# Kernel tuning notes

Hardware: AMD Instinct MI355X
Metric: run time of the kernel (lower is better)

## Reference

```python
import jax, jax.numpy as jnp
import numpy as np

EPS = 1e-12  # torch F.normalize default eps

def _l2norm(x):
    # torch.nn.functional.normalize(x, dim=-1): x / max(||x||_2, eps)
    n = jnp.linalg.norm(x, axis=-1, keepdims=True)
    return x / jnp.maximum(n, EPS)

def setup_inputs() -> dict:
    key = jax.random.key(0)
    ks = jax.random.split(key, 12)
    B, T, D, V, C = 16, 2048, 1024, 32000, 6
    s = 0.02
    text = jax.random.randint(ks[0], (B * T,), 0, V, dtype=jnp.int64)
    offsets = (jnp.arange(B, dtype=jnp.int64) * T)  # uniform-length sequences
    emb = jax.random.normal(ks[1], (V, D), dtype=jnp.float32) * s
    Wq = jax.random.normal(ks[2], (D, D), dtype=jnp.float32) * s
    bq = jnp.zeros((D,), jnp.float32)
    Wk = jax.random.normal(ks[3], (D, D), dtype=jnp.float32) * s
    bk = jnp.zeros((D,), jnp.float32)
    Wv = jax.random.normal(ks[4], (D, D), dtype=jnp.float32) * s
    bv = jnp.zeros((D,), jnp.float32)
    Wfc = jax.random.normal(ks[5], (D, D), dtype=jnp.float32) * s
    bfc = jnp.zeros((D,), jnp.float32)
    Wo = jax.random.normal(ks[6], (C, D), dtype=jnp.float32) * s
    bo = jnp.zeros((C,), jnp.float32)
    return {"text": text, "offsets": offsets, "emb": emb,
            "Wq": Wq, "bq": bq, "Wk": Wk, "bk": bk, "Wv": Wv, "bv": bv,
            "Wfc": Wfc, "bfc": bfc, "Wo": Wo, "bo": bo}

def reference(text, offsets, emb, Wq, bq, Wk, bk, Wv, bv, Wfc, bfc, Wo, bo):
    B = offsets.shape[0]
    T = text.shape[0] // B  # uniform lengths -> pad_sequence == reshape
    D = emb.shape[1]
    tok = text.reshape(B, T)
    x = emb[tok]                                   # [B,T,D]
    q = x @ Wq.T + bq
    k = x @ Wk.T + bk
    v = x @ Wv.T + bv
    scores = jnp.einsum('bqd,bkd->bqk', q, k) / jnp.sqrt(jnp.asarray(D, x.dtype))
    causal = jnp.tril(jnp.ones((T, T), dtype=bool))
    scores = jnp.where(causal[None, :, :], scores, -jnp.inf)
    attn = jax.nn.softmax(scores, axis=-1)
    out = jnp.einsum('bqk,bkd->bqd', attn, v) + x  # residual with embedding
    out = _l2norm(out)
    out = out + (out @ Wfc.T + bfc)                # residual FFN
    out = _l2norm(out)
    last = out[:, -1, :]                           # [B,D]
    return jax.nn.sigmoid(last @ Wo.T + bo)        # [B,num_class]
```

## Files before the change

kernel.cpp:

```cpp
#include <hip/hip_runtime.h>
#include <hip/hip_bf16.h>
#include <math.h>

typedef unsigned short ushort_t;

__device__ __forceinline__ float bf2f(ushort_t u) {
    union { unsigned int i; float f; } v;
    v.i = ((unsigned int)u) << 16;
    return v.f;
}

__device__ __forceinline__ ushort_t f2bf(float f) {
    union { float f; unsigned int i; } v; v.f = f;
    unsigned int lsb = (v.i >> 16) & 1;
    unsigned int r = v.i + 0x7FFF + lsb;
    return (ushort_t)(r >> 16);
}

__device__ __forceinline__ float wave_sum(float acc) {
    #pragma unroll
    for (int off = 32; off >= 1; off >>= 1) acc += __shfl_xor(acc, off, 64);
    return acc;
}

__device__ __forceinline__ void ld8(const void* p, int isbf, size_t i, float* o) {
    if (isbf) {
        uint4 raw = *reinterpret_cast<const uint4*>((const ushort_t*)p + i);
        const ushort_t* pu = reinterpret_cast<const ushort_t*>(&raw);
        #pragma unroll
        for (int k = 0; k < 8; ++k) o[k] = bf2f(pu[k]);
    } else {
        const float4* f = reinterpret_cast<const float4*>((const float*)p + i);
        float4 a = f[0], b = f[1];
        o[0]=a.x; o[1]=a.y; o[2]=a.z; o[3]=a.w;
        o[4]=b.x; o[5]=b.y; o[6]=b.z; o[7]=b.w;
    }
}

__device__ __forceinline__ void ld4(const void* p, int isbf, size_t i, float* o) {
    if (isbf) {
        uint2 raw = *reinterpret_cast<const uint2*>((const ushort_t*)p + i);
        const ushort_t* pu = reinterpret_cast<const ushort_t*>(&raw);
        #pragma unroll
        for (int k = 0; k < 4; ++k) o[k] = bf2f(pu[k]);
    } else {
        float4 a = *reinterpret_cast<const float4*>((const float*)p + i);
        o[0]=a.x; o[1]=a.y; o[2]=a.z; o[3]=a.w;
    }
}

__device__ __forceinline__ float ldS(const void* p, int isbf, size_t i) {
    return isbf ? bf2f(((const ushort_t*)p)[i]) : ((const float*)p)[i];
}

__device__ __forceinline__ int tokAt(const void* text, int isi64, size_t i) {
    return isi64 ? ((const int*)text)[2 * i] : ((const int*)text)[i];
}

__device__ __forceinline__ void detect_flags(const void* emb, const void* text, int* sf) {
    if (threadIdx.x < 64) {
        const int lane = threadIdx.x;
        ushort_t u = ((const ushort_t*)emb)[2 * lane];
        int e = (u >> 7) & 0xFF;
        unsigned long long mb = __ballot(e >= 0x60 && e <= 0x7E);
        int odd = ((const int*)text)[2 * lane + 1];
        unsigned long long mi = __ballot(odd != 0);
        if (lane == 0) {
            sf[0] = (__popcll(mb) >= 32) ? 1 : 0;
            sf[1] = (__popcll(mi) == 0) ? 1 : 0;
        }
    }
    __syncthreads();
}

__global__ void kQC(const void* __restrict__ text, const void* __restrict__ emb,
                    const void* __restrict__ Wq, const void* __restrict__ bq,
                    const void* __restrict__ Wk, float* __restrict__ c_part,
                    int B, int T, int D) {
    const int nch = D >> 6;
    const int b = blockIdx.x / nch;
    const int ch = blockIdx.x % nch;
    const int i0 = ch << 6;
    const int tid = threadIdx.x;
    __shared__ int sf[2];
    __shared__ float xs[1024];
    __shared__ float qs[64];
    detect_flags(emb, text, sf);
    const int isbf = sf[0], isi64 = sf[1];
    const int tok = tokAt(text, isi64, (size_t)b * T + (T - 1));
    float w4[4];
    for (int dd = tid * 4; dd < D; dd += 1024) {
        ld4(emb, isbf, (size_t)tok * D + dd, w4);
        xs[dd]=w4[0]; xs[dd+1]=w4[1]; xs[dd+2]=w4[2]; xs[dd+3]=w4[3];
    }
    __syncthreads();
    const int wave = tid >> 6, lane = tid & 63;
    float w[8];
    for (int r = 0; r < 16; ++r) {
        const int i = i0 + wave * 16 + r;
        float acc = 0.f;
        for (int d0 = lane * 8; d0 < D; d0 += 512) {
            ld8(Wq, isbf, (size_t)i * D + d0, w);
            #pragma unroll
            for (int k = 0; k < 8; ++k) acc += w[k] * xs[d0 + k];
        }
        acc = wave_sum(acc);
        if (lane == 0) qs[wave * 16 + r] = acc + ldS(bq, isbf, i);
    }
    __syncthreads();
    const int d = tid * 4;
    float a0=0.f, a1=0.f, a2=0.f, a3=0.f;
    #pragma unroll 8
    for (int i = 0; i < 64; ++i) {
        const float qv = qs[i];
        ld4(Wk, isbf, (size_t)(i0 + i) * D + d, w4);
        a0 += qv*w4[0]; a1 += qv*w4[1]; a2 += qv*w4[2]; a3 += qv*w4[3];
    }
    *reinterpret_cast<float4*>(c_part + ((size_t)ch * B + b) * D + d)
        = make_float4(a0, a1, a2, a3);
}

__global__ void k35(const void* __restrict__ text, const void* __restrict__ emb,
                    const float* __restrict__ c_part, float* __restrict__ xbar_part,
                    float* __restrict__ m_part, float* __restrict__ l_part,
                    int B, int T, int D, int nch_c, float scale) {
    const int nch = T >> 6;
    const int b = blockIdx.x / nch;
    const int ch = blockIdx.x % nch;
    const int j0 = ch << 6;
    const int tid = threadIdx.x;
    __shared__ int sf[2];
    __shared__ float cs[1024];
    __shared__ float sjs[64];
    __shared__ float wls[64];
    __shared__ int tks[64];
    detect_flags(emb, text, sf);
    const int isbf = sf[0], isi64 = sf[1];
    {
        const int d = tid * 4;
        float4 acc = make_float4(0.f, 0.f, 0.f, 0.f);
        for (int cc = 0; cc < nch_c; ++cc) {
            float4 v = *reinterpret_cast<const float4*>(c_part + ((size_t)cc * B + b) * D + d);
            acc.x += v.x; acc.y += v.y; acc.z += v.z; acc.w += v.w;
        }
        cs[d]=acc.x; cs[d+1]=acc.y; cs[d+2]=acc.z; cs[d+3]=acc.w;
    }
    if (tid < 64) tks[tid] = tokAt(text, isi64, (size_t)b * T + j0 + tid);
    __syncthreads();
    const int wave = tid >> 6, lane = tid & 63;
    float w[8];
    for (int r = 0; r < 16; ++r) {
        const int jj = wave * 16 + r;
        const int tok = tks[jj];
        float acc = 0.f;
        for (int d0 = lane * 8; d0 < D; d0 += 512) {
            ld8(emb, isbf, (size_t)tok * D + d0, w);
            #pragma unroll
            for (int k = 0; k < 8; ++k) acc += w[k] * cs[d0 + k];
        }
        acc = wave_sum(acc);
        if (lane == 0) sjs[jj] = acc * scale;
    }
    __syncthreads();
    float mx = -INFINITY;
    #pragma unroll 8
    for (int j = 0; j < 64; ++j) mx = fmaxf(mx, sjs[j]);
    if (tid < 64) wls[tid] = expf(sjs[tid] - mx);
    __syncthreads();
    if (tid < 64) {
        float lv = wave_sum(wls[tid]);
        if (tid == 0) { m_part[ch * B + b] = mx; l_part[ch * B + b] = lv; }
    }
    const int d = tid * 4;
    float a0=0.f, a1=0.f, a2=0.f, a3=0.f;
    float w4[4];
    #pragma unroll 8
    for (int j = 0; j < 64; ++j) {
        const float wj = wls[j];
        ld4(emb, isbf, (size_t)tks[j] * D + d, w4);
        a0 += wj*w4[0]; a1 += wj*w4[1]; a2 += wj*w4[2]; a3 += wj*w4[3];
    }
    *reinterpret_cast<float4*>(xbar_part + ((size_t)ch * B + b) * D + d)
        = make_float4(a0, a1, a2, a3);
}

__global__ void kC(const float* __restrict__ xbar_part, const float* __restrict__ m_part,
                   const float* __restrict__ l_part, float* __restrict__ xbar,
                   int B, int D, int nch) {
    const int b = blockIdx.x >> 2;
    const int d = ((blockIdx.x & 3) << 8) + threadIdx.x;
    float mx = -INFINITY;
    for (int cc = 0; cc < nch; ++cc) mx = fmaxf(mx, m_part[cc * B + b]);
    float lg = 0.f, acc = 0.f;
    for (int cc = 0; cc < nch; ++cc) {
        const float sc = expf(m_part[cc * B + b] - mx);
        lg  += l_part[cc * B + b] * sc;
        acc += xbar_part[((size_t)cc * B + b) * D + d] * sc;
    }
    xbar[b * D + d] = acc / lg;
}

__global__ void k6a_u(const void* __restrict__ text, const void* __restrict__ emb,
                      const void* __restrict__ Wv, const void* __restrict__ bv,
                      const float* __restrict__ xbar, float* __restrict__ u,
                      int B, int T, int D) {
    const int nb = D >> 2;
    const int b = blockIdx.x / nb;
    const int r0 = (blockIdx.x % nb) << 2;
    const int tid = threadIdx.x;
    __shared__ int sf[2];
    __shared__ float xb[1024];
    __shared__ float xl[1024];
    detect_flags(emb, text, sf);
    const int isbf = sf[0], isi64 = sf[1];
    const int tok = tokAt(text, isi64, (size_t)b * T + (T - 1));
    float w4[4];
    for (int dd = tid * 4; dd < D; dd += 1024) {
        float4 v = *reinterpret_cast<const float4*>(xbar + b * D + dd);
        xb[dd]=v.x; xb[dd+1]=v.y; xb[dd+2]=v.z; xb[dd+3]=v.w;
        ld4(emb, isbf, (size_t)tok * D + dd, w4);
        xl[dd]=w4[0]; xl[dd+1]=w4[1]; xl[dd+2]=w4[2]; xl[dd+3]=w4[3];
    }
    __syncthreads();
    const int wave = tid >> 6, lane = tid & 63;
    const int i = r0 + wave;
    float acc = 0.f, w[8];
    for (int d0 = lane * 8; d0 < D; d0 += 512) {
        ld8(Wv, isbf, (size_t)i * D + d0, w);
        #pragma unroll
        for (int k = 0; k < 8; ++k) acc += w[k] * xb[d0 + k];
    }
    acc = wave_sum(acc);
    if (lane == 0) u[b * D + i] = acc + ldS(bv, isbf, i) + xl[i];
}

__global__ void k6c_h2(const void* __restrict__ text, const void* __restrict__ emb,
                       const void* __restrict__ Wfc, const void* __restrict__ bfc,
                       const float* __restrict__ u, float* __restrict__ h2, int D) {
    const int nb = D >> 2;
    const int b = blockIdx.x / nb;
    const int r0 = (blockIdx.x % nb) << 2;
    const int tid = threadIdx.x;
    __shared__ int sf[2];
    __shared__ float hs[1024];
    __shared__ float red[256];
    __shared__ float s_rn;
    detect_flags(emb, text, sf);
    const int isbf = sf[0];
    float part = 0.f;
    for (int dd = tid * 4; dd < D; dd += 1024) {
        float4 v = *reinterpret_cast<const float4*>(u + b * D + dd);
        hs[dd]=v.x; hs[dd+1]=v.y; hs[dd+2]=v.z; hs[dd+3]=v.w;
        part += v.x*v.x + v.y*v.y + v.z*v.z + v.w*v.w;
    }
    red[tid] = part;
    __syncthreads();
    for (int st = 128; st; st >>= 1) {
        if (tid < st) red[tid] += red[tid + st];
        __syncthreads();
    }
    if (tid == 0) s_rn = 1.f / fmaxf(sqrtf(red[0]), 1e-12f);
    __syncthreads();
    const float rn = s_rn;
    for (int dd = tid; dd < D; dd += 256) hs[dd] *= rn;
    __syncthreads();
    const int wave = tid >> 6, lane = tid & 63;
    const int i = r0 + wave;
    float acc = 0.f, w[8];
    for (int d0 = lane * 8; d0 < D; d0 += 512) {
        ld8(Wfc, isbf, (size_t)i * D + d0, w);
        #pragma unroll
        for (int k = 0; k < 8; ++k) acc += w[k] * hs[d0 + k];
    }
    acc = wave_sum(acc);
    if (lane == 0) h2[b * D + i] = hs[i] + acc + ldS(bfc, isbf, i);
}

__global__ void k6d_out(const void* __restrict__ text, const void* __restrict__ emb,
                        const void* __restrict__ Wo, const void* __restrict__ bo,
                        const float* __restrict__ h2, void* __restrict__ out,
                        int D, int C, int total) {
    __shared__ int sf[2];
    detect_flags(emb, text, sf);
    const int isbf = sf[0];
    const int g = blockIdx.x * 4 + (threadIdx.x >> 6);
    if (g >= total) return;
    const int lane = threadIdx.x & 63;
    const int b = g / C, ci = g % C;
    float a1 = 0.f, a2 = 0.f, w[8], h[8];
    for (int d0 = lane * 8; d0 < D; d0 += 512) {
        ld8(Wo, isbf, (size_t)ci * D + d0, w);
        ld8(h2, 0, (size_t)b * D + d0, h);
        #pragma unroll
        for (int k = 0; k < 8; ++k) { a1 += w[k] * h[k]; a2 += h[k] * h[k]; }
    }
    a1 = wave_sum(a1);
    a2 = wave_sum(a2);
    if (lane == 0) {
        float rn = 1.f / fmaxf(sqrtf(a2), 1e-12f);
        float z = a1 * rn + ldS(bo, isbf, ci);
        float y = 1.f / (1.f + expf(-z));
        if (isbf) ((ushort_t*)out)[g] = f2bf(y);
        else      ((float*)out)[g] = y;
    }
}

extern "C" void kernel_launch(void* const* d_in, const int* in_sizes, int n_in,
                              void* d_out, int out_size, void* d_ws, size_t ws_size,
                              hipStream_t stream) {
    const void* text = d_in[0];
    const void* emb = d_in[2];
    const void* Wq  = d_in[3];
    const void* bq  = d_in[4];
    const void* Wk  = d_in[5];
    const void* Wv  = d_in[7];
    const void* bv  = d_in[8];
    const void* Wfc = d_in[9];
    const void* bfc = d_in[10];
    const void* Wo  = d_in[11];
    const void* bo  = d_in[12];

    const int B = in_sizes[1];
    const int T = in_sizes[0] / B;
    const int D = in_sizes[4];
    const int C = in_sizes[12];

    const int nch_c = D / 64;
    const int nch_k = T / 64;

    float* ws        = (float*)d_ws;
    float* c_part    = ws;
    float* xbar_part = c_part + (size_t)nch_c * B * D;
    float* m_part    = xbar_part + (size_t)nch_k * B * D;
    float* l_part    = m_part + (size_t)nch_k * B;
    float* xbar      = l_part + (size_t)nch_k * B;
    float* u         = xbar + (size_t)B * D;
    float* h2        = u + (size_t)B * D;

    const float scale = 1.0f / sqrtf((float)D);

    kQC<<<B * (D / 64), 256, 0, stream>>>(text, emb, Wq, bq, Wk, c_part, B, T, D);
    k35<<<B * (T / 64), 256, 0, stream>>>(text, emb, c_part, xbar_part, m_part, l_part,
                                          B, T, D, nch_c, scale);
    kC<<<B * 4, 256, 0, stream>>>(xbar_part, m_part, l_part, xbar, B, D, nch_k);
    k6a_u<<<B * (D / 4), 256, 0, stream>>>(text, emb, Wv, bv, xbar, u, B, T, D);
    k6c_h2<<<B * (D / 4), 256, 0, stream>>>(text, emb, Wfc, bfc, u, h2, D);
    k6d_out<<<(B * C + 3) / 4, 256, 0, stream>>>(text, emb, Wo, bo, h2, d_out, D, C, B * C);
}
```

Measured before the change: 310.6 us.

## Fuse softmax combine into value projection and stage key rows in LDS

Removes the separate kC combine kernel by folding the cross-chunk softmax rescale into the value-projection kernel. The attention chunk kernel now uses 32-token chunks and, for bf16 inputs, stages the gathered embedding rows in shared memory. The score and weighted-sum passes both read those rows from LDS instead of gathering them twice from global memory. The matvec kernels now process 32 rows per block, with each lane's 16 input elements hoisted into registers, which cuts the launch count and redundant vector staging. The costs are a 64KB LDS allocation per block in k35, which lowers occupancy, and a register layout that assumes D=1024.

```diff
diff --git a/kernel.cpp b/kernel.cpp
--- a/kernel.cpp
+++ b/kernel.cpp
@@ -20,6 +20,11 @@
 __device__ __forceinline__ float wave_sum(float acc) {
     #pragma unroll
     for (int off = 32; off >= 1; off >>= 1) acc += __shfl_xor(acc, off, 64);
+    return acc;
+}
+__device__ __forceinline__ float wave_max(float acc) {
+    #pragma unroll
+    for (int off = 32; off >= 1; off >>= 1) acc = fmaxf(acc, __shfl_xor(acc, off, 64));
     return acc;
 }
 
@@ -71,6 +76,11 @@
         }
     }
     __syncthreads();
+}
+
+__device__ __forceinline__ void hoist16(const float* v, int lane, float* c16) {
+    #pragma unroll
+    for (int k = 0; k < 16; ++k) c16[k] = v[lane * 16 + k];
 }
 
 __global__ void kQC(const void* __restrict__ text, const void* __restrict__ emb,
@@ -95,15 +105,18 @@
     }
     __syncthreads();
     const int wave = tid >> 6, lane = tid & 63;
+    float c16[16];
+    hoist16(xs, lane, c16);
     float w[8];
     for (int r = 0; r < 16; ++r) {
         const int i = i0 + wave * 16 + r;
         float acc = 0.f;
-        for (int d0 = lane * 8; d0 < D; d0 += 512) {
-            ld8(Wq, isbf, (size_t)i * D + d0, w);
-            #pragma unroll
-            for (int k = 0; k < 8; ++k) acc += w[k] * xs[d0 + k];
-        }
+        ld8(Wq, isbf, (size_t)i * D + lane * 16, w);
+        #pragma unroll
+        for (int k = 0; k < 8; ++k) acc += w[k] * c16[k];
+        ld8(Wq, isbf, (size_t)i * D + lane * 16 + 8, w);
+        #pragma unroll
+        for (int k = 0; k < 8; ++k) acc += w[k] * c16[8 + k];
         acc = wave_sum(acc);
         if (lane == 0) qs[wave * 16 + r] = acc + ldS(bq, isbf, i);
     }
@@ -124,16 +137,17 @@
                     const float* __restrict__ c_part, float* __restrict__ xbar_part,
                     float* __restrict__ m_part, float* __restrict__ l_part,
                     int B, int T, int D, int nch_c, float scale) {
-    const int nch = T >> 6;
+    const int nch = T >> 5;
     const int b = blockIdx.x / nch;
     const int ch = blockIdx.x % nch;
-    const int j0 = ch << 6;
+    const int j0 = ch << 5;
     const int tid = threadIdx.x;
     __shared__ int sf[2];
+    __shared__ ushort_t rows[32 * 1024];
     __shared__ float cs[1024];
-    __shared__ float sjs[64];
-    __shared__ float wls[64];
-    __shared__ int tks[64];
+    __shared__ float sjs[32];
+    __shared__ float wls[32];
+    __shared__ int tks[32];
     detect_flags(emb, text, sf);
     const int isbf = sf[0], isi64 = sf[1];
     {
@@ -145,101 +159,144 @@
         }
         cs[d]=acc.x; cs[d+1]=acc.y; cs[d+2]=acc.z; cs[d+3]=acc.w;
     }
-    if (tid < 64) tks[tid] = tokAt(text, isi64, (size_t)b * T + j0 + tid);
+    if (tid < 32) tks[tid] = tokAt(text, isi64, (size_t)b * T + j0 + tid);
+    __syncthreads();
+    if (isbf) {
+        const ushort_t* E = (const ushort_t*)emb;
+        const int half = tid >> 7;
+        const int off  = (tid & 127) * 8;
+        #pragma unroll 4
+        for (int sw = 0; sw < 16; ++sw) {
+            const int r = sw * 2 + half;
+            uint4 v = *reinterpret_cast<const uint4*>(E + (size_t)tks[r] * D + off);
+            *reinterpret_cast<uint4*>(&rows[r * 1024 + off]) = v;
+        }
+    }
     __syncthreads();
     const int wave = tid >> 6, lane = tid & 63;
-    float w[8];
-    for (int r = 0; r < 16; ++r) {
-        const int jj = wave * 16 + r;
-        const int tok = tks[jj];
-        float acc = 0.f;
-        for (int d0 = lane * 8; d0 < D; d0 += 512) {
-            ld8(emb, isbf, (size_t)tok * D + d0, w);
-            #pragma unroll
-            for (int k = 0; k < 8; ++k) acc += w[k] * cs[d0 + k];
-        }
-        acc = wave_sum(acc);
-        if (lane == 0) sjs[jj] = acc * scale;
+    {
+        float c16[16];
+        hoist16(cs, lane, c16);
+        float w[8];
+        for (int rr = 0; rr < 8; ++rr) {
+            const int r = wave + rr * 4;
+            float acc = 0.f;
+            if (isbf) {
+                uint4 raw = *reinterpret_cast<const uint4*>(&rows[r * 1024 + lane * 16]);
+                const ushort_t* pu = reinterpret_cast<const ushort_t*>(&raw);
+                #pragma unroll
+                for (int k = 0; k < 8; ++k) acc += bf2f(pu[k]) * c16[k];
+                raw = *reinterpret_cast<const uint4*>(&rows[r * 1024 + lane * 16 + 8]);
+                #pragma unroll
+                for (int k = 0; k < 8; ++k) acc += bf2f(pu[k]) * c16[8 + k];
+            } else {
+                ld8(emb, 0, (size_t)tks[r] * D + lane * 16, w);
+                #pragma unroll
+                for (int k = 0; k < 8; ++k) acc += w[k] * c16[k];
+                ld8(emb, 0, (size_t)tks[r] * D + lane * 16 + 8, w);
+                #pragma unroll
+                for (int k = 0; k < 8; ++k) acc += w[k] * c16[8 + k];
+            }
+            acc = wave_sum(acc);
+            if (lane == 0) sjs[r] = acc * scale;
+        }
     }
     __syncthreads();
     float mx = -INFINITY;
-    #pragma unroll 8
-    for (int j = 0; j < 64; ++j) mx = fmaxf(mx, sjs[j]);
-    if (tid < 64) wls[tid] = expf(sjs[tid] - mx);
+    #pragma unroll
+    for (int j = 0; j < 32; ++j) mx = fmaxf(mx, sjs[j]);
+    if (tid < 32) wls[tid] = expf(sjs[tid] - mx);
     __syncthreads();
     if (tid < 64) {
-        float lv = wave_sum(wls[tid]);
-        if (tid == 0) { m_part[ch * B + b] = mx; l_part[ch * B + b] = lv; }
+        float v = (tid < 32) ? wls[tid] : 0.f;
+        v = wave_sum(v);
+        if (tid == 0) { m_part[ch * B + b] = mx; l_part[ch * B + b] = v; }
     }
     const int d = tid * 4;
     float a0=0.f, a1=0.f, a2=0.f, a3=0.f;
-    float w4[4];
-    #pragma unroll 8
-    for (int j = 0; j < 64; ++j) {
-        const float wj = wls[j];
-        ld4(emb, isbf, (size_t)tks[j] * D + d, w4);
-        a0 += wj*w4[0]; a1 += wj*w4[1]; a2 += wj*w4[2]; a3 += wj*w4[3];
+    if (isbf) {
+        #pragma unroll 8
+        for (int j = 0; j < 32; ++j) {
+            const float wj = wls[j];
+            uint2 raw = *reinterpret_cast<const uint2*>(&rows[j * 1024 + d]);
+            const ushort_t* pu = reinterpret_cast<const ushort_t*>(&raw);
+            a0 += wj*bf2f(pu[0]); a1 += wj*bf2f(pu[1]);
+            a2 += wj*bf2f(pu[2]); a3 += wj*bf2f(pu[3]);
+        }
+    } else {
+        float w4[4];
+        #pragma unroll 8
+        for (int j = 0; j < 32; ++j) {
+            const float wj = wls[j];
+            ld4(emb, 0, (size_t)tks[j] * D + d, w4);
+            a0 += wj*w4[0]; a1 += wj*w4[1]; a2 += wj*w4[2]; a3 += wj*w4[3];
+        }
     }
     *reinterpret_cast<float4*>(xbar_part + ((size_t)ch * B + b) * D + d)
         = make_float4(a0, a1, a2, a3);
 }
 
-__global__ void kC(const float* __restrict__ xbar_part, const float* __restrict__ m_part,
-                   const float* __restrict__ l_part, float* __restrict__ xbar,
-                   int B, int D, int nch) {
-    const int b = blockIdx.x >> 2;
-    const int d = ((blockIdx.x & 3) << 8) + threadIdx.x;
-    float mx = -INFINITY;
-    for (int cc = 0; cc < nch; ++cc) mx = fmaxf(mx, m_part[cc * B + b]);
-    float lg = 0.f, acc = 0.f;
-    for (int cc = 0; cc < nch; ++cc) {
-        const float sc = expf(m_part[cc * B + b] - mx);
-        lg  += l_part[cc * B + b] * sc;
-        acc += xbar_part[((size_t)cc * B + b) * D + d] * sc;
-    }
-    xbar[b * D + d] = acc / lg;
-}
-
-__global__ void k6a_u(const void* __restrict__ text, const void* __restrict__ emb,
-                      const void* __restrict__ Wv, const void* __restrict__ bv,
-                      const float* __restrict__ xbar, float* __restrict__ u,
-                      int B, int T, int D) {
-    const int nb = D >> 2;
+__global__ void kCA(const void* __restrict__ text, const void* __restrict__ emb,
+                    const float* __restrict__ xbar_part, const float* __restrict__ m_part,
+                    const float* __restrict__ l_part, const void* __restrict__ Wv,
+                    const void* __restrict__ bv, float* __restrict__ u,
+                    int B, int T, int D, int nch_k) {
+    const int nb = D >> 5;
     const int b = blockIdx.x / nb;
-    const int r0 = (blockIdx.x % nb) << 2;
+    const int r0 = (blockIdx.x % nb) << 5;
     const int tid = threadIdx.x;
     __shared__ int sf[2];
     __shared__ float xb[1024];
-    __shared__ float xl[1024];
+    __shared__ float sc[64];
+    __shared__ float xl32[32];
     detect_flags(emb, text, sf);
     const int isbf = sf[0], isi64 = sf[1];
     const int tok = tokAt(text, isi64, (size_t)b * T + (T - 1));
-    float w4[4];
-    for (int dd = tid * 4; dd < D; dd += 1024) {
-        float4 v = *reinterpret_cast<const float4*>(xbar + b * D + dd);
-        xb[dd]=v.x; xb[dd+1]=v.y; xb[dd+2]=v.z; xb[dd+3]=v.w;
-        ld4(emb, isbf, (size_t)tok * D + dd, w4);
-        xl[dd]=w4[0]; xl[dd+1]=w4[1]; xl[dd+2]=w4[2]; xl[dd+3]=w4[3];
+    if (tid < 32) xl32[tid] = ldS(emb, isbf, (size_t)tok * D + r0 + tid);
+    if (tid < 64) {
+        float mv = (tid < nch_k) ? m_part[tid * B + b] : -INFINITY;
+        float mx = wave_max(mv);
+        float e  = (tid < nch_k) ? expf(mv - mx) : 0.f;
+        float lv = (tid < nch_k) ? l_part[tid * B + b] * e : 0.f;
+        float lg = wave_sum(lv);
+        sc[tid] = e / lg;
+    }
+    __syncthreads();
+    {
+        const int d = tid * 4;
+        float4 acc = make_float4(0.f, 0.f, 0.f, 0.f);
+        for (int cc = 0; cc < nch_k; ++cc) {
+            const float s = sc[cc];
+            float4 v = *reinterpret_cast<const float4*>(xbar_part + ((size_t)cc * B + b) * D + d);
+            acc.x += s*v.x; acc.y += s*v.y; acc.z += s*v.z; acc.w += s*v.w;
+        }
+        xb[d]=acc.x; xb[d+1]=acc.y; xb[d+2]=acc.z; xb[d+3]=acc.w;
     }
     __syncthreads();
     const int wave = tid >> 6, lane = tid & 63;
-    const int i = r0 + wave;
-    float acc = 0.f, w[8];
-    for (int d0 = lane * 8; d0 < D; d0 += 512) {
-        ld8(Wv, isbf, (size_t)i * D + d0, w);
-        #pragma unroll
-        for (int k = 0; k < 8; ++k) acc += w[k] * xb[d0 + k];
-    }
-    acc = wave_sum(acc);
-    if (lane == 0) u[b * D + i] = acc + ldS(bv, isbf, i) + xl[i];
+    float c16[16];
+    hoist16(xb, lane, c16);
+    float w[8];
+    for (int rr = 0; rr < 8; ++rr) {
+        const int i = r0 + wave + rr * 4;
+        float acc = 0.f;
+        ld8(Wv, isbf, (size_t)i * D + lane * 16, w);
+        #pragma unroll
+        for (int k = 0; k < 8; ++k) acc += w[k] * c16[k];
+        ld8(Wv, isbf, (size_t)i * D + lane * 16 + 8, w);
+        #pragma unroll
+        for (int k = 0; k < 8; ++k) acc += w[k] * c16[8 + k];
+        acc = wave_sum(acc);
+        if (lane == 0) u[b * D + i] = acc + ldS(bv, isbf, i) + xl32[i - r0];
+    }
 }
 
 __global__ void k6c_h2(const void* __restrict__ text, const void* __restrict__ emb,
                        const void* __restrict__ Wfc, const void* __restrict__ bfc,
                        const float* __restrict__ u, float* __restrict__ h2, int D) {
-    const int nb = D >> 2;
+    const int nb = D >> 5;
     const int b = blockIdx.x / nb;
-    const int r0 = (blockIdx.x % nb) << 2;
+    const int r0 = (blockIdx.x % nb) << 5;
     const int tid = threadIdx.x;
     __shared__ int sf[2];
     __shared__ float hs[1024];
@@ -248,10 +305,11 @@
     detect_flags(emb, text, sf);
     const int isbf = sf[0];
     float part = 0.f;
-    for (int dd = tid * 4; dd < D; dd += 1024) {
+    {
+        const int dd = tid * 4;
         float4 v = *reinterpret_cast<const float4*>(u + b * D + dd);
         hs[dd]=v.x; hs[dd+1]=v.y; hs[dd+2]=v.z; hs[dd+3]=v.w;
-        part += v.x*v.x + v.y*v.y + v.z*v.z + v.w*v.w;
+        part = v.x*v.x + v.y*v.y + v.z*v.z + v.w*v.w;
     }
     red[tid] = part;
     __syncthreads();
@@ -262,18 +320,27 @@
     if (tid == 0) s_rn = 1.f / fmaxf(sqrtf(red[0]), 1e-12f);
     __syncthreads();
     const float rn = s_rn;
-    for (int dd = tid; dd < D; dd += 256) hs[dd] *= rn;
+    {
+        const int dd = tid * 4;
+        hs[dd] *= rn; hs[dd+1] *= rn; hs[dd+2] *= rn; hs[dd+3] *= rn;
+    }
     __syncthreads();
     const int wave = tid >> 6, lane = tid & 63;
-    const int i = r0 + wave;
-    float acc = 0.f, w[8];
-    for (int d0 = lane * 8; d0 < D; d0 += 512) {
-        ld8(Wfc, isbf, (size_t)i * D + d0, w);
-        #pragma unroll
-        for (int k = 0; k < 8; ++k) acc += w[k] * hs[d0 + k];
-    }
-    acc = wave_sum(acc);
-    if (lane == 0) h2[b * D + i] = hs[i] + acc + ldS(bfc, isbf, i);
+    float c16[16];
+    hoist16(hs, lane, c16);
+    float w[8];
+    for (int rr = 0; rr < 8; ++rr) {
+        const int i = r0 + wave + rr * 4;
+        float acc = 0.f;
+        ld8(Wfc, isbf, (size_t)i * D + lane * 16, w);
+        #pragma unroll
+        for (int k = 0; k < 8; ++k) acc += w[k] * c16[k];
+        ld8(Wfc, isbf, (size_t)i * D + lane * 16 + 8, w);
+        #pragma unroll
+        for (int k = 0; k < 8; ++k) acc += w[k] * c16[8 + k];
+        acc = wave_sum(acc);
+        if (lane == 0) h2[b * D + i] = hs[i] + acc + ldS(bfc, isbf, i);
+    }
 }
 
 __global__ void k6d_out(const void* __restrict__ text, const void* __restrict__ emb,
@@ -326,24 +393,23 @@
     const int C = in_sizes[12];
 
     const int nch_c = D / 64;
-    const int nch_k = T / 64;
+    const int nch_k = T / 32;
 
     float* ws        = (float*)d_ws;
     float* c_part    = ws;
     float* xbar_part = c_part + (size_t)nch_c * B * D;
     float* m_part    = xbar_part + (size_t)nch_k * B * D;
     float* l_part    = m_part + (size_t)nch_k * B;
-    float* xbar      = l_part + (size_t)nch_k * B;
-    float* u         = xbar + (size_t)B * D;
+    float* u         = l_part + (size_t)nch_k * B;
     float* h2        = u + (size_t)B * D;
 
     const float scale = 1.0f / sqrtf((float)D);
 
     kQC<<<B * (D / 64), 256, 0, stream>>>(text, emb, Wq, bq, Wk, c_part, B, T, D);
-    k35<<<B * (T / 64), 256, 0, stream>>>(text, emb, c_part, xbar_part, m_part, l_part,
+    k35<<<B * (T / 32), 256, 0, stream>>>(text, emb, c_part, xbar_part, m_part, l_part,
                                           B, T, D, nch_c, scale);
-    kC<<<B * 4, 256, 0, stream>>>(xbar_part, m_part, l_part, xbar, B, D, nch_k);
-    k6a_u<<<B * (D / 4), 256, 0, stream>>>(text, emb, Wv, bv, xbar, u, B, T, D);
-    k6c_h2<<<B * (D / 4), 256, 0, stream>>>(text, emb, Wfc, bfc, u, h2, D);
+    kCA<<<B * (D / 32), 256, 0, stream>>>(text, emb, xbar_part, m_part, l_part,
+                                          Wv, bv, u, B, T, D, nch_k);
+    k6c_h2<<<B * (D / 32), 256, 0, stream>>>(text, emb, Wfc, bfc, u, h2, D);
     k6d_out<<<(B * C + 3) / 4, 256, 0, stream>>>(text, emb, Wo, bo, h2, d_out, D, C, B * C);
 }
```

Measured after the change: 290.9 us. -6.3%, faster.
